# Performance work log

Measured on AMD Instinct MI355X. Metric: run time of the kernel, lower is better.

## Reference

```python
import jax, jax.numpy as jnp
import numpy as np

TAU = 0.07
COS_EPS = 1e-8   # torch F.cosine_similarity eps
L1_EPS = 1e-12   # torch F.normalize eps
MM_EPS = 1e-8    # min-max renorm eps

B, C, H, W = 64, 256, 32, 32
S, D = 512, 256


def setup_inputs() -> dict:
    key = jax.random.key(0)
    k1, k2, k3, k4 = jax.random.split(key, 4)
    scale = 1.0 / np.sqrt(D)
    return {
        "image_patches": jax.random.normal(k1, (B, C, H, W), dtype=jnp.float32),
        "text_tokens": jax.random.normal(k2, (B, S, D), dtype=jnp.float32),
        "Wv": jax.random.normal(k3, (D, D), dtype=jnp.float32) * scale,
        "bv": jnp.zeros((D,), dtype=jnp.float32),
        "Wt": jax.random.normal(k4, (D, D), dtype=jnp.float32) * scale,
        "bt": jnp.zeros((D,), dtype=jnp.float32),
    }


def _linear(x, Wgt, b):
    return x @ Wgt.T + b


def _l2n(x, axis=-1):
    n = jnp.maximum(jnp.linalg.norm(x, axis=axis, keepdims=True), COS_EPS)
    return x / n


def _sym_ce_diag(sim):
    # sim [..., N, N]; mean of -log_softmax diagonals along both class axes
    lsm_r = jax.nn.log_softmax(sim, axis=-1)
    lsm_c = jax.nn.log_softmax(sim, axis=-2)
    d_r = jnp.diagonal(lsm_r, axis1=-2, axis2=-1)
    d_c = jnp.diagonal(lsm_c, axis1=-2, axis2=-1)
    return 0.5 * (-jnp.mean(d_r) - jnp.mean(d_c))


def reference(image_patches, text_tokens, Wv, bv, Wt, bt):
    b, c, h, w = image_patches.shape
    hw = h * w
    # b c h w -> b (h w) c, then adapters
    patches = image_patches.reshape(b, c, hw).transpose(0, 2, 1)  # [b, hw, c]
    patches = _linear(patches, Wv, bv)          # [b, hw, d]
    tokens = _linear(text_tokens, Wt, bt)       # [b, s, d]

    # global embeddings: mean-pool then adapter (adapter applied twice on vision path)
    g_img = _linear(jnp.mean(patches, axis=1), Wv, bv)  # [b, d]
    g_txt = _linear(jnp.mean(tokens, axis=1), Wt, bt)   # [b, d]

    # global contrastive loss (cosine sim / tau, symmetric CE over batch)
    g_sim = (_l2n(g_img) @ _l2n(g_txt).T) / TAU         # [b, b]
    global_loss = _sym_ce_diag(g_sim)

    # fine-grained alignment
    sim = jnp.einsum('bpd,bsd->bps', patches, tokens)   # [b, hw, s]
    mn = jnp.min(sim, axis=1, keepdims=True)
    mx = jnp.max(sim, axis=1, keepdims=True)
    sim = (sim - mn) / (mx - mn + MM_EPS)
    sigma = 1.0 / hw
    sim = jnp.where(sim < sigma, 0.0, sim)
    # L1 normalize over patch dim (torch F.normalize p=1 dim=1)
    weights = sim / jnp.maximum(jnp.sum(jnp.abs(sim), axis=1, keepdims=True), L1_EPS)
    lgve = jnp.einsum('bps,bpd->bsd', weights, patches)  # [b, s, d]

    # fine-grained contrastive loss: cosine sim between grouped-vision and text tokens
    f_sim = jnp.einsum('bid,bjd->bij', _l2n(lgve), _l2n(tokens)) / TAU  # [b, s, s]
    fine_loss = _sym_ce_diag(f_sim)

    return global_loss + fine_loss
```

## Files before the change

kernel.cpp:

```cpp
#include <hip/hip_runtime.h>
#include <math.h>

#define BB   64
#define HWP  1024
#define SS   512
#define DD   256
#define TAU_INV (1.0f/0.07f)
#define SIGMA   (1.0f/1024.0f)

typedef unsigned short us;
typedef __attribute__((ext_vector_type(8))) short short8v;
typedef __attribute__((ext_vector_type(8))) unsigned short ushort8v;
typedef __attribute__((ext_vector_type(4))) float floatx4;

__device__ __forceinline__ float bf2f(us u) {
    return __uint_as_float((unsigned)u << 16);
}
__device__ __forceinline__ us f2bf(float f) {
    unsigned u = __float_as_uint(f);
    u += 0x7FFFu + ((u >> 16) & 1u);
    return (us)(u >> 16);
}
__device__ __forceinline__ void split_bf(float v, us& h, us& l) {
    h = f2bf(v);
    l = f2bf(v - bf2f(h));
}

__device__ __forceinline__ void dma16(const us* g, us* l) {
    __builtin_amdgcn_global_load_lds(
        (const __attribute__((address_space(1))) unsigned int*)g,
        (__attribute__((address_space(3))) unsigned int*)l, 16, 0, 0);
}

__global__ void zero_out_k(float* out) { if (threadIdx.x == 0) out[0] = 0.0f; }

enum { OPM_F32_ROW = 0, OPM_F32_COL = 1, OPM_SPL_ROW = 2, OPM_SPL_COL = 3,
       OPM_B16_COL = 4, OPM_B16_ROW = 5, OPM_WGT_COL = 6, OPM_WGT_ROW = 7 };
enum { OUT_F32 = 0, OUT_B16 = 1 };

#define LDSTRIDE 40

template<int MODE, int ROWS, int NW>
struct SRegs {
    static constexpr int RR = ROWS / 128;
    static constexpr bool ISF32 = (MODE == OPM_F32_ROW) || (MODE == OPM_F32_COL);
    ushort8v h[ISF32 ? 1 : RR][2];
    ushort8v l[(MODE == OPM_SPL_ROW) ? RR : 1][2];
    float4   f[ISF32 ? RR : 1][4];
};

template<int MODE, int ROWS, int NW>
__device__ __forceinline__ void stage_load(
    const char* p0, const char* p1, int ld, int row0, int k0, int tid,
    SRegs<MODE, ROWS, NW>& R)
{
    #pragma unroll
    for (int rr = 0; rr < ROWS / 128; ++rr) {
        if constexpr (MODE == OPM_SPL_ROW) {
            const us* ph = (const us*)p0;
            const us* pl = (const us*)p1;
            if constexpr (NW == 4) {
                const int i = rr * 128 + (tid >> 1), ko = (tid & 1) * 16;
                const long long g = (long long)(row0 + i) * ld + k0 + ko;
                R.h[rr][0] = *(const ushort8v*)&ph[g];
                R.h[rr][1] = *(const ushort8v*)&ph[g + 8];
                R.l[rr][0] = *(const ushort8v*)&pl[g];
                R.l[rr][1] = *(const ushort8v*)&pl[g + 8];
            } else {
                const int i = rr * 128 + (tid >> 2), ko = (tid & 3) * 8;
                const long long g = (long long)(row0 + i) * ld + k0 + ko;
                R.h[rr][0] = *(const ushort8v*)&ph[g];
                R.l[rr][0] = *(const ushort8v*)&pl[g];
            }
        } else if constexpr (MODE == OPM_B16_ROW || MODE == OPM_WGT_ROW) {
            const us* ph = (const us*)p0;
            if constexpr (NW == 4) {
                const int i = rr * 128 + (tid >> 1), ko = (tid & 1) * 16;
                const long long g = (long long)(row0 + i) * ld + k0 + ko;
                R.h[rr][0] = *(const ushort8v*)&ph[g];
                R.h[rr][1] = *(const ushort8v*)&ph[g + 8];
            } else {
                const int i = rr * 128 + (tid >> 2), ko = (tid & 3) * 8;
                const long long g = (long long)(row0 + i) * ld + k0 + ko;
                R.h[rr][0] = *(const ushort8v*)&ph[g];
            }
        } else if constexpr (MODE == OPM_F32_ROW) {
            const float* pf = (const float*)p0;
            if constexpr (NW == 4) {
                const int i = rr * 128 + (tid >> 1), ko = (tid & 1) * 16;
                const long long g = (long long)(row0 + i) * ld + k0 + ko;
                #pragma unroll
                for (int c = 0; c < 4; ++c)
                    R.f[rr][c] = *(const float4*)&pf[g + c * 4];
            } else {
                const int i = rr * 128 + (tid >> 2), ko = (tid & 3) * 8;
                const long long g = (long long)(row0 + i) * ld + k0 + ko;
                R.f[rr][0] = *(const float4*)&pf[g];
                R.f[rr][1] = *(const float4*)&pf[g + 4];
            }
        } else if constexpr (MODE == OPM_F32_COL) {
            const float* pf = (const float*)p0;
            if constexpr (NW == 4) {
                const int m = rr * 128 + (tid & 127), kh = (tid >> 7) * 16;
                const long long base = (long long)(k0 + kh) * ld + row0 + m;
                #pragma unroll
                for (int c = 0; c < 4; ++c) {
                    float4 v;
                    v.x = pf[base + (long long)(c * 4 + 0) * ld];
                    v.y = pf[base + (long long)(c * 4 + 1) * ld];
                    v.z = pf[base + (long long)(c * 4 + 2) * ld];
                    v.w = pf[base + (long long)(c * 4 + 3) * ld];
                    R.f[rr][c] = v;
                }
            } else {
                const int m = rr * 128 + (tid & 127), kh = (tid >> 7) * 8;
                const long long base = (long long)(k0 + kh) * ld + row0 + m;
                #pragma unroll
                for (int c = 0; c < 2; ++c) {
                    float4 v;
                    v.x = pf[base + (long long)(c * 4 + 0) * ld];
                    v.y = pf[base + (long long)(c * 4 + 1) * ld];
                    v.z = pf[base + (long long)(c * 4 + 2) * ld];
                    v.w = pf[base + (long long)(c * 4 + 3) * ld];
                    R.f[rr][c] = v;
                }
            }
        } else if constexpr (MODE == OPM_B16_COL) {
            const us* ph = (const us*)p0;
            if constexpr (NW == 4) {
                const int m = rr * 128 + (tid & 127), kh = (tid >> 7) * 16;
                const long long base = (long long)(k0 + kh) * ld + row0 + m;
                #pragma unroll
                for (int kk = 0; kk < 8; ++kk) {
                    R.h[rr][0][kk] = ph[base + (long long)kk * ld];
                    R.h[rr][1][kk] = ph[base + (long long)(kk + 8) * ld];
                }
            } else {
                const int m = rr * 128 + (tid & 127), kh = (tid >> 7) * 8;
                const long long base = (long long)(k0 + kh) * ld + row0 + m;
                #pragma unroll
                for (int kk = 0; kk < 8; ++kk)
                    R.h[rr][0][kk] = ph[base + (long long)kk * ld];
            }
        }
    }
}

template<int MODE, int ROWS, int NW>
__device__ __forceinline__ void stage_store(
    const SRegs<MODE, ROWS, NW>& R, us* ldsH, us* ldsL, int tid, float nlo, float inv)
{
    #pragma unroll
    for (int rr = 0; rr < ROWS / 128; ++rr) {
        if constexpr (MODE == OPM_SPL_ROW) {
            if constexpr (NW == 4) {
                const int i = rr * 128 + (tid >> 1), ko = (tid & 1) * 16;
                *(ushort8v*)&ldsH[i * LDSTRIDE + ko]     = R.h[rr][0];
                *(ushort8v*)&ldsH[i * LDSTRIDE + ko + 8] = R.h[rr][1];
                *(ushort8v*)&ldsL[i * LDSTRIDE + ko]     = R.l[rr][0];
                *(ushort8v*)&ldsL[i * LDSTRIDE + ko + 8] = R.l[rr][1];
            } else {
                const int i = rr * 128 + (tid >> 2), ko = (tid & 3) * 8;
                *(ushort8v*)&ldsH[i * LDSTRIDE + ko] = R.h[rr][0];
                *(ushort8v*)&ldsL[i * LDSTRIDE + ko] = R.l[rr][0];
            }
        } else if constexpr (MODE == OPM_B16_ROW) {
            if constexpr (NW == 4) {
                const int i = rr * 128 + (tid >> 1), ko = (tid & 1) * 16;
                *(ushort8v*)&ldsH[i * LDSTRIDE + ko]     = R.h[rr][0];
                *(ushort8v*)&ldsH[i * LDSTRIDE + ko + 8] = R.h[rr][1];
            } else {
                const int i = rr * 128 + (tid >> 2), ko = (tid & 3) * 8;
                *(ushort8v*)&ldsH[i * LDSTRIDE + ko] = R.h[rr][0];
            }
        } else if constexpr (MODE == OPM_WGT_ROW) {
            const int i = tid >> 2, ko = (tid & 3) * 8;
            us v[8];
            #pragma unroll
            for (int j = 0; j < 8; ++j) {
                const float w0 = fmaf(bf2f(R.h[0][0][j]), inv, nlo);
                v[j] = (w0 < SIGMA) ? (us)0 : f2bf(w0);
            }
            *(ushort8v*)&ldsH[i * LDSTRIDE + ko] = *(const ushort8v*)&v[0];
        } else if constexpr (MODE == OPM_F32_ROW) {
            if constexpr (NW == 4) {
                const int i = rr * 128 + (tid >> 1), ko = (tid & 1) * 16;
                us h16[16], l16a[16];
                #pragma unroll
                for (int c = 0; c < 4; ++c) {
                    float4 v = R.f[rr][c];
                    split_bf(v.x, h16[c*4+0], l16a[c*4+0]);
                    split_bf(v.y, h16[c*4+1], l16a[c*4+1]);
                    split_bf(v.z, h16[c*4+2], l16a[c*4+2]);
                    split_bf(v.w, h16[c*4+3], l16a[c*4+3]);
                }
                *(ushort8v*)&ldsH[i * LDSTRIDE + ko]     = *(const ushort8v*)&h16[0];
                *(ushort8v*)&ldsH[i * LDSTRIDE + ko + 8] = *(const ushort8v*)&h16[8];
                *(ushort8v*)&ldsL[i * LDSTRIDE + ko]     = *(const ushort8v*)&l16a[0];
                *(ushort8v*)&ldsL[i * LDSTRIDE + ko + 8] = *(const ushort8v*)&l16a[8];
            } else {
                const int i = rr * 128 + (tid >> 2), ko = (tid & 3) * 8;
                us h8[8], l8[8];
                #pragma unroll
                for (int c = 0; c < 2; ++c) {
                    float4 v = R.f[rr][c];
                    split_bf(v.x, h8[c*4+0], l8[c*4+0]);
                    split_bf(v.y, h8[c*4+1], l8[c*4+1]);
                    split_bf(v.z, h8[c*4+2], l8[c*4+2]);
                    split_bf(v.w, h8[c*4+3], l8[c*4+3]);
                }
                *(ushort8v*)&ldsH[i * LDSTRIDE + ko] = *(const ushort8v*)&h8[0];
                *(ushort8v*)&ldsL[i * LDSTRIDE + ko] = *(const ushort8v*)&l8[0];
            }
        } else if constexpr (MODE == OPM_F32_COL) {
            if constexpr (NW == 4) {
                const int m = rr * 128 + (tid & 127), kh = (tid >> 7) * 16;
                us vh[16], vl[16];
                #pragma unroll
                for (int c = 0; c < 4; ++c) {
                    float4 v = R.f[rr][c];
                    split_bf(v.x, vh[c*4+0], vl[c*4+0]);
                    split_bf(v.y, vh[c*4+1], vl[c*4+1]);
                    split_bf(v.z, vh[c*4+2], vl[c*4+2]);
                    split_bf(v.w, vh[c*4+3], vl[c*4+3]);
                }
                *(ushort8v*)&ldsH[m * LDSTRIDE + kh]     = *(const ushort8v*)&vh[0];
                *(ushort8v*)&ldsH[m * LDSTRIDE + kh + 8] = *(const ushort8v*)&vh[8];
                *(ushort8v*)&ldsL[m * LDSTRIDE + kh]     = *(const ushort8v*)&vl[0];
                *(ushort8v*)&ldsL[m * LDSTRIDE + kh + 8] = *(const ushort8v*)&vl[8];
            } else {
                const int m = rr * 128 + (tid & 127), kh = (tid >> 7) * 8;
                us vh[8], vl[8];
                #pragma unroll
                for (int c = 0; c < 2; ++c) {
                    float4 v = R.f[rr][c];
                    split_bf(v.x, vh[c*4+0], vl[c*4+0]);
                    split_bf(v.y, vh[c*4+1], vl[c*4+1]);
                    split_bf(v.z, vh[c*4+2], vl[c*4+2]);
                    split_bf(v.w, vh[c*4+3], vl[c*4+3]);
                }
                *(ushort8v*)&ldsH[m * LDSTRIDE + kh] = *(const ushort8v*)&vh[0];
                *(ushort8v*)&ldsL[m * LDSTRIDE + kh] = *(const ushort8v*)&vl[0];
            }
        } else if constexpr (MODE == OPM_B16_COL) {
            if constexpr (NW == 4) {
                const int m = rr * 128 + (tid & 127), kh = (tid >> 7) * 16;
                us v[16];
                #pragma unroll
                for (int kk = 0; kk < 16; ++kk)
                    v[kk] = (kk < 8) ? R.h[rr][0][kk & 7] : R.h[rr][1][kk & 7];
                *(ushort8v*)&ldsH[m * LDSTRIDE + kh]     = *(const ushort8v*)&v[0];
                *(ushort8v*)&ldsH[m * LDSTRIDE + kh + 8] = *(const ushort8v*)&v[8];
            } else {
                const int m = rr * 128 + (tid & 127), kh = (tid >> 7) * 8;
                *(ushort8v*)&ldsH[m * LDSTRIDE + kh] = R.h[rr][0];
            }
        }
    }
}

template<int AMODE, int BMODE, int OMODE, int EPI, int NT, int PREF, int NW, int DMA>
__global__ __launch_bounds__(NW * 64) void mfma_gemm(
    const void* A0, const void* A1, const void* B0, const void* B1, void* C0,
    int M, int N, int K, int lda, int ldb, int ldc,
    long long sA, long long sB, long long sC,
    const float* __restrict__ bias, const float* __restrict__ invm,
    const float* __restrict__ invn, float scale,
    const float* __restrict__ wlo, const float* __restrict__ whi,
    float* __restrict__ aux0, float* __restrict__ aux1,
    float* __restrict__ aux2, float* __restrict__ aux3, float* __restrict__ aux4)
{
    constexpr bool ASPL = (AMODE <= OPM_SPL_COL);
    constexpr bool BSPL = (BMODE <= OPM_SPL_COL);
    constexpr int NF = NT / 16;
    constexpr int MI = 8 / NW;
    constexpr int RPW = 128 / NW;
    __shared__ __align__(16) us Ah[(DMA == 1) ? 8 : 128 * LDSTRIDE];
    __shared__ __align__(16) us Al[(!DMA && ASPL) ? 128 * LDSTRIDE : 8];
    __shared__ __align__(16) us Bh[DMA ? 8 : NT * LDSTRIDE];
    __shared__ __align__(16) us Bl[(!DMA && BSPL) ? NT * LDSTRIDE : 8];
    __shared__ __align__(16) us AhD[(DMA == 1) ? 2 * 128 * 32 : 8];
    __shared__ __align__(16) us BhD[DMA ? 2 * NT * 32 : 8];
    __shared__ float redm[(EPI == 4) ? NW * NT : 1];
    __shared__ float reds[(EPI == 4) ? NW * NT : 1];

    const int tid = threadIdx.x;
    const int w = tid >> 6, lane = tid & 63;
    const int quad = lane >> 4, l16 = lane & 15;

    int bx = blockIdx.x, by = blockIdx.y, bz = blockIdx.z;
    {
        const int nbx = gridDim.x, nby = gridDim.y, nbz = gridDim.z;
        const int nwg = nbx * nby * nbz;
        if ((nwg & 7) == 0) {
            const int hw = bx + nbx * (by + nby * bz);
            const int cpx = nwg >> 3;
            int wk = (hw & 7) * cpx + (hw >> 3);
            bx = wk % nbx; wk /= nbx;
            by = wk % nby; bz = wk / nby;
        }
    }

    const int m0 = bx * 128, n0 = by * NT;
    const int b = bz;

    const char* Ab0 = (const char*)A0 + (long long)b * sA;
    const char* Ab1 = A1 ? (const char*)A1 + (long long)b * sA : nullptr;
    const char* Bb0 = (const char*)B0 + (long long)b * sB;
    const char* Bb1 = B1 ? (const char*)B1 + (long long)b * sB : nullptr;

    floatx4 acc[MI][NF];
    #pragma unroll
    for (int mi = 0; mi < MI; ++mi)
        #pragma unroll
        for (int ni = 0; ni < NF; ++ni)
            acc[mi][ni] = (floatx4){0.f, 0.f, 0.f, 0.f};

    if constexpr (DMA == 1) {
        const us* Abu = (const us*)Ab0;
        const us* Bbu = (const us*)Bb0;
        const int drow = 16 * w + (lane >> 2);
        const int dcol = (lane & 3) * 8;
        const us* aS = Abu + (long long)(m0 + drow) * lda + dcol;
        const us* bS = Bbu + (long long)(n0 + drow) * ldb + dcol;
        us* aD = &AhD[0] + 512 * w;
        us* bD = &BhD[0] + 512 * w;
        const int NTL = K >> 5;

        dma16(aS,      aD);
        dma16(bS,      bD);
        dma16(aS + 32, aD + 128 * 32);
        dma16(bS + 32, bD + NT * 32);

        int cur = 0;
        for (int t = 0; t < NTL; ++t) {
            if (t + 1 == NTL) asm volatile("s_waitcnt vmcnt(0)" ::: "memory");
            else              asm volatile("s_waitcnt vmcnt(2)" ::: "memory");
            __builtin_amdgcn_s_barrier();
            asm volatile("" ::: "memory");

            {
                const us* Ac = &AhD[cur * 128 * 32];
                const us* Bc = &BhD[cur * NT * 32];
                short8v ah = *(const short8v*)&Ac[(16 * w + l16) * 32 + quad * 8];
                #pragma unroll
                for (int ni = 0; ni < NF; ++ni) {
                    short8v bh = *(const short8v*)&Bc[(16 * ni + l16) * 32 + quad * 8];
                    acc[0][ni] = __builtin_amdgcn_mfma_f32_16x16x32_bf16(ah, bh, acc[0][ni], 0, 0, 0);
                }
            }

            asm volatile("" ::: "memory");
            __builtin_amdgcn_s_barrier();
            if (t + 2 < NTL) {
                const long long off = (long long)(t + 2) * 32;
                dma16(aS + off, aD + cur * 128 * 32);
                dma16(bS + off, bD + cur * NT * 32);
            }
            cur ^= 1;
        }
    } else if constexpr (DMA == 2) {
        const us* Abu = (const us*)Ab0;
        const us* Bbu = (const us*)Bb0;
        const float* wloA = wlo + (long long)b * M;
        const float* whiA = whi + (long long)b * M;
        const int ai = tid >> 2, ako = (tid & 3) * 8;
        const float lo = wloA[m0 + ai];
        const float invA = 1.0f / (whiA[m0 + ai] - lo + 1e-8f);
        const float nloA = -lo * invA;

        const int rB = 16 * w + (lane >> 2);
        const us* bS = Bbu + (long long)(n0 + rB) * ldb + (lane & 3) * 8;
        us* bD = &BhD[0] + 512 * w;
        const long long aRow = (long long)(m0 + ai) * lda + ako;
        const int NTL = K >> 5;

        dma16(bS, bD);
        ushort8v ra = *(const ushort8v*)&Abu[aRow];
        dma16(bS + 32, bD + 4096);

        int cur = 0;
        for (int t = 0; t < NTL; ++t) {
            us v[8];
            #pragma unroll
            for (int j = 0; j < 8; ++j) {
                const float w0 = fmaf(bf2f(ra[j]), invA, nloA);
                v[j] = (w0 < SIGMA) ? (us)0 : f2bf(w0);
            }
            *(ushort8v*)&Ah[ai * LDSTRIDE + ako] = *(const ushort8v*)&v[0];
            asm volatile("s_waitcnt vmcnt(1) lgkmcnt(0)" ::: "memory");
            __builtin_amdgcn_s_barrier();

            if (t + 1 < NTL)
                ra = *(const ushort8v*)&Abu[aRow + (long long)(t + 1) * 32];

            {
                const us* Bc = &BhD[cur * 4096];
                short8v ah = *(const short8v*)&Ah[(16 * w + l16) * LDSTRIDE + quad * 8];
                #pragma unroll
                for (int ni = 0; ni < NF; ++ni) {
                    short8v bh = *(const short8v*)&Bc[(16 * ni + l16) * 32 + quad * 8];
                    acc[0][ni] = __builtin_amdgcn_mfma_f32_16x16x32_bf16(ah, bh, acc[0][ni], 0, 0, 0);
                }
            }
            asm volatile("" ::: "memory");
            __builtin_amdgcn_s_barrier();
            if (t + 2 < NTL)
                dma16(bS + (long long)(t + 2) * 32, bD + cur * 4096);
            cur ^= 1;
        }
    } else {
        float nloA = 0.f, invA = 0.f;
        if constexpr (AMODE == OPM_WGT_ROW) {
            const float* wloA = wlo + (long long)b * M;
            const float* whiA = whi + (long long)b * M;
            const int row = m0 + (tid >> 2);
            const float lo = wloA[row];
            invA = 1.0f / (whiA[row] - lo + 1e-8f);
            nloA = -lo * invA;
        }

        SRegs<AMODE, 128, NW> RA0, RA1;
        SRegs<BMODE, NT, NW>  RB0, RB1;
        if constexpr (PREF) {
            stage_load<AMODE, 128, NW>(Ab0, Ab1, lda, m0, 0, tid, RA0);
            stage_load<BMODE, NT, NW>(Bb0, Bb1, ldb, n0, 0, tid, RB0);
            stage_load<AMODE, 128, NW>(Ab0, Ab1, lda, m0, 32, tid, RA1);
            stage_load<BMODE, NT, NW>(Bb0, Bb1, ldb, n0, 32, tid, RB1);
        }

        auto do_mfma = [&]() {
            short8v ah[MI], al[MI];
            #pragma unroll
            for (int mi = 0; mi < MI; ++mi) {
                const int r = (RPW * w + 16 * mi + l16) * LDSTRIDE + quad * 8;
                ah[mi] = *(const short8v*)&Ah[r];
                if constexpr (ASPL) al[mi] = *(const short8v*)&Al[r];
            }
            #pragma unroll
            for (int ni = 0; ni < NF; ++ni) {
                const int rB = (16 * ni + l16) * LDSTRIDE + quad * 8;
                short8v bh = *(const short8v*)&Bh[rB];
                #pragma unroll
                for (int mi = 0; mi < MI; ++mi)
                    acc[mi][ni] = __builtin_amdgcn_mfma_f32_16x16x32_bf16(ah[mi], bh, acc[mi][ni], 0, 0, 0);
                if constexpr (BSPL) {
                    short8v bl = *(const short8v*)&Bl[rB];
                    #pragma unroll
                    for (int mi = 0; mi < MI; ++mi)
                        acc[mi][ni] = __builtin_amdgcn_mfma_f32_16x16x32_bf16(ah[mi], bl, acc[mi][ni], 0, 0, 0);
                }
                if constexpr (ASPL) {
                    #pragma unroll
                    for (int mi = 0; mi < MI; ++mi)
                        acc[mi][ni] = __builtin_amdgcn_mfma_f32_16x16x32_bf16(al[mi], bh, acc[mi][ni], 0, 0, 0);
                }
            }
        };

#define GEMM_SUBSTEP(RAx, RBx, KCUR, KNEXT)                                    \
    do {                                                                       \
        if constexpr (!PREF) {                                                 \
            stage_load<AMODE, 128, NW>(Ab0, Ab1, lda, m0, (KCUR), tid, RAx);   \
            stage_load<BMODE, NT, NW>(Bb0, Bb1, ldb, n0, (KCUR), tid, RBx);    \
        }                                                                      \
        stage_store<AMODE, 128, NW>(RAx, Ah, Al, tid, nloA, invA);             \
        stage_store<BMODE, NT, NW>(RBx, Bh, Bl, tid, 0.f, 0.f);                \
        if constexpr (PREF) {                                                  \
            asm volatile("s_waitcnt lgkmcnt(0)" ::: "memory");                 \
            __builtin_amdgcn_s_barrier();                                      \
            if ((KNEXT) < K) {                                                 \
                stage_load<AMODE, 128, NW>(Ab0, Ab1, lda, m0, (KNEXT), tid, RAx); \
                stage_load<BMODE, NT, NW>(Bb0, Bb1, ldb, n0, (KNEXT), tid, RBx);  \
            }                                                                  \
        } else {                                                               \
            __syncthreads();                                                   \
        }                                                                      \
        do_mfma();                                                             \
        if constexpr (PREF) {                                                  \
            asm volatile("s_waitcnt lgkmcnt(0)" ::: "memory");                 \
            __builtin_amdgcn_s_barrier();                                      \
        } else {                                                               \
            __syncthreads();                                                   \
        }                                                                      \
    } while (0)

        for (int k0 = 0; k0 < K; k0 += 64) {
            GEMM_SUBSTEP(RA0, RB0, k0, k0 + 64);
            GEMM_SUBSTEP(RA1, RB1, k0 + 32, k0 + 96);
        }
#undef GEMM_SUBSTEP
    }

    if constexpr (EPI != 4) {
        char* Cb0 = (char*)C0 + (long long)b * sC;
        #pragma unroll
        for (int mi = 0; mi < MI; ++mi)
            #pragma unroll
            for (int ni = 0; ni < NF; ++ni)
                #pragma unroll
                for (int r = 0; r < 4; ++r) {
                    const int row = m0 + RPW * w + 16 * mi + quad * 4 + r;
                    const int col = n0 + 16 * ni + l16;
                    float v = acc[mi][ni][r];
                    if constexpr (EPI == 1) v += bias[col];
                    const long long idx = (long long)row * ldc + col;
                    if constexpr (OMODE == OUT_F32) ((float*)Cb0)[idx] = v;
                    else                            ((us*)Cb0)[idx] = f2bf(v);
                }
    }

    if constexpr (EPI == 3) {
        #pragma unroll
        for (int r = 0; r < 4; ++r) {
            const int grow = m0 + RPW * w + quad * 4 + r;
            float lo = 1e30f, hi = -1e30f;
            #pragma unroll
            for (int ni = 0; ni < NF; ++ni) {
                const float vr = bf2f(f2bf(acc[0][ni][r]));
                lo = fminf(lo, vr); hi = fmaxf(hi, vr);
            }
            lo = fminf(lo, __shfl_xor(lo, 1)); hi = fmaxf(hi, __shfl_xor(hi, 1));
            lo = fminf(lo, __shfl_xor(lo, 2)); hi = fmaxf(hi, __shfl_xor(hi, 2));
            lo = fminf(lo, __shfl_xor(lo, 4)); hi = fmaxf(hi, __shfl_xor(hi, 4));
            lo = fminf(lo, __shfl_xor(lo, 8)); hi = fmaxf(hi, __shfl_xor(hi, 8));
            if (l16 == 0) {
                const long long o = ((long long)b * M + grow) * 8 + by;
                aux0[o] = lo; aux1[o] = hi;
            }
        }
    }

    if constexpr (EPI == 4) {
        float bn[NF];
        #pragma unroll
        for (int ni = 0; ni < NF; ++ni)
            bn[ni] = invn[(long long)b * N + n0 + 16 * ni + l16] * scale;
        float amv[MI * 4];
        #pragma unroll
        for (int mi = 0; mi < MI; ++mi)
            #pragma unroll
            for (int r = 0; r < 4; ++r)
                amv[mi * 4 + r] = invm[(long long)b * M + m0 + RPW * w + 16 * mi + quad * 4 + r];

        #pragma unroll
        for (int mi = 0; mi < MI; ++mi)
            #pragma unroll
            for (int r = 0; r < 4; ++r) {
                const int grow = m0 + RPW * w + 16 * mi + quad * 4 + r;
                float vv[NF];
                float rm = -1e30f;
                #pragma unroll
                for (int ni = 0; ni < NF; ++ni) {
                    const float v = acc[mi][ni][r] * amv[mi * 4 + r] * bn[ni];
                    vv[ni] = v;
                    rm = fmaxf(rm, v);
                    if (grow == n0 + 16 * ni + l16)
                        aux4[(long long)b * M + grow] = v;
                }
                #pragma unroll
                for (int o = 8; o > 0; o >>= 1) rm = fmaxf(rm, __shfl_xor(rm, o));
                float rs = 0.f;
                #pragma unroll
                for (int ni = 0; ni < NF; ++ni) rs += expf(vv[ni] - rm);
                #pragma unroll
                for (int o = 8; o > 0; o >>= 1) rs += __shfl_xor(rs, o);
                if (l16 == 0) {
                    const long long o = ((long long)b * M + grow) * 4 + by;
                    aux0[o] = rm; aux1[o] = rs;
                }
            }

        #pragma unroll
        for (int ni = 0; ni < NF; ++ni) {
            float va[MI * 4];
            float cm = -1e30f;
            #pragma unroll
            for (int mi = 0; mi < MI; ++mi)
                #pragma unroll
                for (int r = 0; r < 4; ++r) {
                    const float v = acc[mi][ni][r] * amv[mi * 4 + r] * bn[ni];
                    va[mi * 4 + r] = v;
                    cm = fmaxf(cm, v);
                }
            cm = fmaxf(cm, __shfl_xor(cm, 16));
            cm = fmaxf(cm, __shfl_xor(cm, 32));
            float cs = 0.f;
            #pragma unroll
            for (int j = 0; j < MI * 4; ++j) cs += expf(va[j] - cm);
            cs += __shfl_xor(cs, 16);
            cs += __shfl_xor(cs, 32);
            if (quad == 0) {
                redm[w * NT + 16 * ni + l16] = cm;
                reds[w * NT + 16 * ni + l16] = cs;
            }
        }
        __syncthreads();
        if (tid < NT) {
            float m = -1e30f, s = 0.f;
            #pragma unroll
            for (int w4 = 0; w4 < NW; ++w4) {
                const float cm = redm[w4 * NT + tid], cs = reds[w4 * NT + tid];
                const float nm = fmaxf(m, cm);
                s = s * expf(m - nm) + cs * expf(cm - nm);
                m = nm;
            }
            const long long o = ((long long)b * N + n0 + tid) * 4 + bx;
            aux2[o] = m; aux3[o] = s;
        }
    }
}


__global__ __launch_bounds__(256) void transpose_k(
    const us* __restrict__ src, us* __restrict__ dst)
{
    __shared__ us t[64][66];
    const int b = blockIdx.z;
    const int p0 = blockIdx.x * 64, d0 = blockIdx.y * 64;
    const us* s = src + (long long)b * 262144;
    us* d = dst + (long long)b * 262144;
    const int r = threadIdx.x >> 3, c8 = (threadIdx.x & 7) * 8;
    #pragma unroll
    for (int h = 0; h < 64; h += 32)
        *(ushort8v*)&t[r + h][c8] =
            *(const ushort8v*)&s[(long long)(p0 + r + h) * 256 + d0 + c8];
    __syncthreads();
    #pragma unroll
    for (int h = 0; h < 64; h += 32) {
        us v[8];
        #pragma unroll
        for (int j = 0; j < 8; ++j) v[j] = t[c8 + j][r + h];
        *(ushort8v*)&d[(long long)(d0 + r + h) * 1024 + p0 + c8] =
            *(const ushort8v*)&v[0];
    }
}

__global__ __launch_bounds__(256) void convert_w_k(
    const float* Wv, const float* Wt, us* Wvh, us* Wvl, us* Wth, us* Wtl)
{
    const int i = blockIdx.x * 256 + threadIdx.x;
    split_bf(Wv[i], Wvh[i], Wvl[i]);
    split_bf(Wt[i], Wth[i], Wtl[i]);
}

__global__ __launch_bounds__(256) void mean_img_k(
    const float* __restrict__ img, float* __restrict__ mimg)
{
    const int row = blockIdx.x * 4 + (threadIdx.x >> 6);
    const int lane = threadIdx.x & 63;
    const float* p = img + (long long)row * 1024;
    float s = 0.f;
    #pragma unroll
    for (int c = 0; c < 4; ++c) {
        float4 v = *(const float4*)&p[(c * 64 + lane) * 4];
        s += v.x + v.y + v.z + v.w;
    }
    #pragma unroll
    for (int o = 32; o > 0; o >>= 1) s += __shfl_xor(s, o);
    if (lane == 0) mimg[row] = s * (1.0f / 1024.0f);
}

__global__ __launch_bounds__(256) void mean_text_s1(
    const float* __restrict__ text, float* __restrict__ part)
{
    const int b = blockIdx.x, ch = blockIdx.y, k = threadIdx.x;
    const float* p = text + ((long long)b * 512 + ch * 64) * 256 + k;
    float s = 0.f;
    for (int r = 0; r < 64; ++r) s += p[r * 256];
    part[(b * 8 + ch) * 256 + k] = s;
}
__global__ __launch_bounds__(256) void mean_text_s2(
    const float* __restrict__ part, float* __restrict__ mt)
{
    const int b = blockIdx.x, k = threadIdx.x;
    float s = 0.f;
    for (int c = 0; c < 8; ++c) s += part[(b * 8 + c) * 256 + k];
    mt[b * 256 + k] = s * (1.0f / 512.0f);
}

__global__ __launch_bounds__(256) void small_adapter_k(
    const float* __restrict__ x, const float* __restrict__ W,
    const float* __restrict__ bias, float* __restrict__ y)
{
    const int b = blockIdx.x, d = threadIdx.x;
    __shared__ float xs[256];
    xs[d] = x[b * 256 + d];
    __syncthreads();
    const float4* w = (const float4*)(W + (long long)d * 256);
    const float4* xv = (const float4*)xs;
    float s = bias[d];
    #pragma unroll 8
    for (int k = 0; k < 64; ++k) {
        const float4 a = xv[k], ww = w[k];
        s += a.x * ww.x + a.y * ww.y + a.z * ww.z + a.w * ww.w;
    }
    y[b * 256 + d] = s;
}


__global__ __launch_bounds__(256) void inv_norm_f32_k(
    const float* __restrict__ x, float* __restrict__ inv)
{
    const int row = blockIdx.x * 4 + (threadIdx.x >> 6);
    const int lane = threadIdx.x & 63;
    float4 v = *(const float4*)&x[(long long)row * 256 + lane * 4];
    float s = v.x * v.x + v.y * v.y + v.z * v.z + v.w * v.w;
    #pragma unroll
    for (int o = 32; o > 0; o >>= 1) s += __shfl_xor(s, o);
    if (lane == 0) inv[row] = 1.0f / fmaxf(sqrtf(s), 1e-8f);
}

__global__ __launch_bounds__(256) void g_sim_k(
    const float* __restrict__ gi, const float* __restrict__ gt,
    const float* __restrict__ invI, const float* __restrict__ invT,
    float* __restrict__ gs)
{
    const int i = blockIdx.x, t = threadIdx.x;
    const int j = t >> 2, part = t & 3;
    __shared__ float a[256];
    a[t] = gi[i * 256 + t];
    __syncthreads();
    const float* bp = gt + (long long)j * 256 + part * 64;
    const float* ap = a + part * 64;
    float s = 0.f;
    #pragma unroll 16
    for (int k = 0; k < 64; ++k) s += ap[k] * bp[k];
    s += __shfl_xor(s, 1);
    s += __shfl_xor(s, 2);
    if (part == 0) gs[i * 64 + j] = s * invI[i] * invT[j] * TAU_INV;
}

__global__ __launch_bounds__(64) void g_lse_k(
    const float* __restrict__ gs, float* __restrict__ out)
{
    const int b = blockIdx.x, lane = threadIdx.x;
    const bool is_col = b >= 64;
    const int r = is_col ? b - 64 : b;
    const float v = is_col ? gs[lane * 64 + r] : gs[r * 64 + lane];
    float m = v;
    #pragma unroll
    for (int o = 32; o > 0; o >>= 1) m = fmaxf(m, __shfl_xor(m, o));
    float s = expf(v - m);
    #pragma unroll
    for (int o = 32; o > 0; o >>= 1) s += __shfl_xor(s, o);
    if (lane == 0)
        atomicAdd(out, ((m + logf(s)) - gs[r * 64 + r]) * (0.5f / 64.0f));
}

__global__ __launch_bounds__(256) void inv_norm_b16_k(
    const us* __restrict__ x, float* __restrict__ inv)
{
    const int row = blockIdx.x * 4 + (threadIdx.x >> 6);
    const int lane = threadIdx.x & 63;
    ushort4 h = *(const ushort4*)&x[(long long)row * 256 + lane * 4];
    const float x0 = bf2f(h.x), x1 = bf2f(h.y), x2 = bf2f(h.z), x3 = bf2f(h.w);
    float s = x0 * x0 + x1 * x1 + x2 * x2 + x3 * x3;
    #pragma unroll
    for (int o = 32; o > 0; o >>= 1) s += __shfl_xor(s, o);
    if (lane == 0) inv[row] = 1.0f / fmaxf(sqrtf(s), 1e-8f);
}


__global__ __launch_bounds__(256) void minmax_merge_k(
    const float* __restrict__ mnp, const float* __restrict__ mxp,
    float* __restrict__ mn, float* __restrict__ mx)
{
    const int idx = blockIdx.x * 256 + threadIdx.x;
    float lo = 1e30f, hi = -1e30f;
    #pragma unroll
    for (int c = 0; c < 8; ++c) {
        lo = fminf(lo, mnp[(long long)idx * 8 + c]);
        hi = fmaxf(hi, mxp[(long long)idx * 8 + c]);
    }
    mn[idx] = lo; mx[idx] = hi;
}

__global__ __launch_bounds__(256) void fine_merge4_k(
    const float* __restrict__ pm, const float* __restrict__ ps,
    const float* __restrict__ diag, float* __restrict__ out)
{
    const int idx = blockIdx.x * 256 + threadIdx.x;
    float m = -1e30f, s = 0.f;
    #pragma unroll
    for (int c = 0; c < 4; ++c) {
        const float cm = pm[(long long)idx * 4 + c], cs = ps[(long long)idx * 4 + c];
        const float nm = fmaxf(m, cm);
        s = s * expf(m - nm) + cs * expf(cm - nm);
        m = nm;
    }
    const float contrib = (m + logf(s)) - diag[idx];
    __shared__ float red[256];
    red[threadIdx.x] = contrib;
    __syncthreads();
    for (int w = 128; w > 0; w >>= 1) {
        if (threadIdx.x < w) red[threadIdx.x] += red[threadIdx.x + w];
        __syncthreads();
    }
    if (threadIdx.x == 0) atomicAdd(out, red[0] * (0.5f / (64.0f * 512.0f)));
}

extern "C" void kernel_launch(void* const* d_in, const int* in_sizes, int n_in,
                              void* d_out, int out_size, void* d_ws, size_t ws_size,
                              hipStream_t stream)
{
    const float* img  = (const float*)d_in[0];
    const float* text = (const float*)d_in[1];
    const float* Wv   = (const float*)d_in[2];
    const float* bv   = (const float*)d_in[3];
    const float* Wt   = (const float*)d_in[4];
    const float* bt   = (const float*)d_in[5];
    float* out = (float*)d_out;
    char* ws = (char*)d_ws;

    us* patches = (us*)(ws + 0);
    us* tokens  = (us*)(ws + 33554432);
    us* simT    = (us*)(ws + 50331648);
    us* lgve    = (us*)(ws + 117440512);
    char* st = ws + 134217728;
    float* mean_img  = (float*)(st + 0);
    float* mean_text = (float*)(st + 65536);
    float* mean_pat  = (float*)(st + 131072);
    float* mean_tok  = (float*)(st + 196608);
    float* g_img     = (float*)(st + 262144);
    float* g_txt     = (float*)(st + 327680);
    float* textpart  = (float*)(st + 393216);
    float* mnp       = (float*)(st + 917504);
    float* mxp       = (float*)(st + 1966080);
    float* mnv       = (float*)(st + 3014656);
    float* mxv       = (float*)(st + 3145728);
    float* inv_l     = (float*)(st + 3276800);
    float* inv_t     = (float*)(st + 3407872);
    us* Wvh = (us*)(st + 3538944);
    us* Wvl = (us*)(st + 3670016);
    us* Wth = (us*)(st + 3801088);
    us* Wtl = (us*)(st + 3932160);
    float* inv_gi  = (float*)(st + 4063232);
    float* inv_gt  = (float*)(st + 4063744);
    float* g_simbf = (float*)(st + 4064256);
    float* pm_row  = (float*)(st + 4194304);
    float* ps_row  = (float*)(st + 4718592);
    float* pm_col  = (float*)(st + 5242880);
    float* ps_col  = (float*)(st + 5767168);
    float* diag    = (float*)(st + 6291456);
    us* patchesT   = (us*)(ws + 140640256);

    zero_out_k<<<1, 64, 0, stream>>>(out);
    convert_w_k<<<256, 256, 0, stream>>>(Wv, Wt, Wvh, Wvl, Wth, Wtl);

    mean_img_k<<<4096, 256, 0, stream>>>(img, mean_img);
    mean_text_s1<<<dim3(64, 8), 256, 0, stream>>>(text, textpart);
    mean_text_s2<<<64, 256, 0, stream>>>(textpart, mean_text);
    small_adapter_k<<<BB, 256, 0, stream>>>(mean_img, Wv, bv, mean_pat);
    small_adapter_k<<<BB, 256, 0, stream>>>(mean_pat, Wv, bv, g_img);
    small_adapter_k<<<BB, 256, 0, stream>>>(mean_text, Wt, bt, mean_tok);
    small_adapter_k<<<BB, 256, 0, stream>>>(mean_tok, Wt, bt, g_txt);
    inv_norm_f32_k<<<16, 256, 0, stream>>>(g_img, inv_gi);
    inv_norm_f32_k<<<16, 256, 0, stream>>>(g_txt, inv_gt);
    g_sim_k<<<64, 256, 0, stream>>>(g_img, g_txt, inv_gi, inv_gt, g_simbf);
    g_lse_k<<<128, 64, 0, stream>>>(g_simbf, out);

    mfma_gemm<OPM_F32_COL, OPM_SPL_ROW, OUT_B16, 1, 256, 0, 8, 0><<<dim3(8, 1, BB), 512, 0, stream>>>(
        img, nullptr, Wvh, Wvl, patches,
        1024, 256, 256, 1024, 256, 256,
        1048576LL, 0LL, 524288LL, bv, nullptr, nullptr, 0.f, nullptr, nullptr,
        nullptr, nullptr, nullptr, nullptr, nullptr);

    mfma_gemm<OPM_F32_ROW, OPM_SPL_ROW, OUT_B16, 1, 256, 0, 8, 0><<<dim3(4, 1, BB), 512, 0, stream>>>(
        text, nullptr, Wth, Wtl, tokens,
        512, 256, 256, 256, 256, 256,
        524288LL, 0LL, 262144LL, bt, nullptr, nullptr, 0.f, nullptr, nullptr,
        nullptr, nullptr, nullptr, nullptr, nullptr);

    transpose_k<<<dim3(16, 4, BB), 256, 0, stream>>>(patches, patchesT);

    mfma_gemm<OPM_B16_ROW, OPM_B16_ROW, OUT_B16, 3, 128, 0, 8, 1><<<dim3(4, 8, BB), 512, 0, stream>>>(
        tokens, nullptr, patches, nullptr, simT,
        512, 1024, 256, 256, 256, 1024,
        262144LL, 524288LL, 1048576LL, nullptr, nullptr, nullptr, 0.f, nullptr, nullptr,
        mnp, mxp, nullptr, nullptr, nullptr);

    minmax_merge_k<<<128, 256, 0, stream>>>(mnp, mxp, mnv, mxv);

    mfma_gemm<OPM_WGT_ROW, OPM_B16_COL, OUT_B16, 0, 128, 0, 8, 2><<<dim3(4, 2, BB), 512, 0, stream>>>(
        simT, nullptr, patchesT, nullptr, lgve,
        512, 256, 1024, 1024, 1024, 256,
        1048576LL, 524288LL, 262144LL, nullptr, nullptr, nullptr, 0.f, mnv, mxv,
        nullptr, nullptr, nullptr, nullptr, nullptr);

    inv_norm_b16_k<<<8192, 256, 0, stream>>>(lgve, inv_l);
    inv_norm_b16_k<<<8192, 256, 0, stream>>>(tokens, inv_t);

    mfma_gemm<OPM_B16_ROW, OPM_B16_ROW, OUT_B16, 4, 128, 0, 8, 1><<<dim3(4, 4, BB), 512, 0, stream>>>(
        lgve, nullptr, tokens, nullptr, nullptr,
        512, 512, 256, 256, 256, 512,
        262144LL, 262144LL, 0LL, nullptr, inv_l, inv_t, TAU_INV, nullptr, nullptr,
        pm_row, ps_row, pm_col, ps_col, diag);

    fine_merge4_k<<<128, 256, 0, stream>>>(pm_row, ps_row, diag, out);
    fine_merge4_k<<<128, 256, 0, stream>>>(pm_col, ps_col, diag, out);
}
```

Baseline: 378.3 us.

## Pre-split adapter inputs to bf16 hi/lo and stream via async DMA GEMM

```diff
diff --git a/kernel.cpp b/kernel.cpp
--- a/kernel.cpp
+++ b/kernel.cpp
@@ -275,12 +275,14 @@
     constexpr int NF = NT / 16;
     constexpr int MI = 8 / NW;
     constexpr int RPW = 128 / NW;
-    __shared__ __align__(16) us Ah[(DMA == 1) ? 8 : 128 * LDSTRIDE];
+    __shared__ __align__(16) us Ah[(DMA == 1 || DMA == 3) ? 8 : 128 * LDSTRIDE];
     __shared__ __align__(16) us Al[(!DMA && ASPL) ? 128 * LDSTRIDE : 8];
     __shared__ __align__(16) us Bh[DMA ? 8 : NT * LDSTRIDE];
     __shared__ __align__(16) us Bl[(!DMA && BSPL) ? NT * LDSTRIDE : 8];
-    __shared__ __align__(16) us AhD[(DMA == 1) ? 2 * 128 * 32 : 8];
+    __shared__ __align__(16) us AhD[(DMA == 1 || DMA == 3) ? 2 * 128 * 32 : 8];
     __shared__ __align__(16) us BhD[DMA ? 2 * NT * 32 : 8];
+    __shared__ __align__(16) us AlD[(DMA == 3) ? 2 * 128 * 32 : 8];
+    __shared__ __align__(16) us BlD[(DMA == 3) ? 2 * NT * 32 : 8];
     __shared__ float redm[(EPI == 4) ? NW * NT : 1];
     __shared__ float reds[(EPI == 4) ? NW * NT : 1];
 
@@ -407,6 +409,64 @@
             __builtin_amdgcn_s_barrier();
             if (t + 2 < NTL)
                 dma16(bS + (long long)(t + 2) * 32, bD + cur * 4096);
+            cur ^= 1;
+        }
+    } else if constexpr (DMA == 3) {
+        const us* AhU = (const us*)Ab0;
+        const us* AlU = (const us*)Ab1;
+        const us* BhU = (const us*)Bb0;
+        const us* BlU = (const us*)Bb1;
+        const int drow = 16 * w + (lane >> 2);
+        const int dcol = (lane & 3) * 8;
+        const us* aHS = AhU + (long long)(m0 + drow) * lda + dcol;
+        const us* aLS = AlU + (long long)(m0 + drow) * lda + dcol;
+        const us* bHS = BhU + (long long)(n0 + drow) * ldb + dcol;
+        const us* bLS = BlU + (long long)(n0 + drow) * ldb + dcol;
+        us* aHDp = &AhD[0] + 512 * w;
+        us* aLDp = &AlD[0] + 512 * w;
+        us* bHDp = &BhD[0] + 512 * w;
+        us* bLDp = &BlD[0] + 512 * w;
+        const int NTL = K >> 5;
+
+        dma16(aHS, aHDp); dma16(aLS, aLDp); dma16(bHS, bHDp); dma16(bLS, bLDp);
+        dma16(aHS + 32, aHDp + 4096); dma16(aLS + 32, aLDp + 4096);
+        dma16(bHS + 32, bHDp + 4096); dma16(bLS + 32, bLDp + 4096);
+
+        int cur = 0;
+        for (int t = 0; t < NTL; ++t) {
+            if (t + 1 == NTL) asm volatile("s_waitcnt vmcnt(0)" ::: "memory");
+            else              asm volatile("s_waitcnt vmcnt(4)" ::: "memory");
+            __builtin_amdgcn_s_barrier();
+            asm volatile("" ::: "memory");
+
+            {
+                const us* Ach = &AhD[cur * 4096];
+                const us* Acl = &AlD[cur * 4096];
+                const us* Bch = &BhD[cur * 4096];
+                const us* Bcl = &BlD[cur * 4096];
+                const int ra = (16 * w + l16) * 32 + quad * 8;
+                short8v ah = *(const short8v*)&Ach[ra];
+                short8v al = *(const short8v*)&Acl[ra];
+                #pragma unroll
+                for (int ni = 0; ni < NF; ++ni) {
+                    const int rb = (16 * ni + l16) * 32 + quad * 8;
+                    short8v bh = *(const short8v*)&Bch[rb];
+                    short8v bl = *(const short8v*)&Bcl[rb];
+                    acc[0][ni] = __builtin_amdgcn_mfma_f32_16x16x32_bf16(ah, bh, acc[0][ni], 0, 0, 0);
+                    acc[0][ni] = __builtin_amdgcn_mfma_f32_16x16x32_bf16(ah, bl, acc[0][ni], 0, 0, 0);
+                    acc[0][ni] = __builtin_amdgcn_mfma_f32_16x16x32_bf16(al, bh, acc[0][ni], 0, 0, 0);
+                }
+            }
+
+            asm volatile("" ::: "memory");
+            __builtin_amdgcn_s_barrier();
+            if (t + 2 < NTL) {
+                const long long off = (long long)(t + 2) * 32;
+                dma16(aHS + off, aHDp + cur * 4096);
+                dma16(aLS + off, aLDp + cur * 4096);
+                dma16(bHS + off, bHDp + cur * 4096);
+                dma16(bLS + off, bLDp + cur * 4096);
+            }
             cur ^= 1;
         }
     } else {
@@ -634,6 +694,46 @@
         *(ushort8v*)&d[(long long)(d0 + r + h) * 1024 + p0 + c8] =
             *(const ushort8v*)&v[0];
     }
+}
+
+__global__ __launch_bounds__(256) void convsplit_img_k(
+    const float* __restrict__ img, us* __restrict__ th, us* __restrict__ tl)
+{
+    __shared__ float t[64][65];
+    const int b = blockIdx.z;
+    const int p0 = blockIdx.x * 64, c0 = blockIdx.y * 64;
+    const float* s = img + (long long)b * 262144;
+    const int r = threadIdx.x >> 4, c4 = (threadIdx.x & 15) * 4;
+    #pragma unroll
+    for (int h = 0; h < 64; h += 16) {
+        float4 v = *(const float4*)&s[(long long)(c0 + r + h) * 1024 + p0 + c4];
+        t[r + h][c4 + 0] = v.x; t[r + h][c4 + 1] = v.y;
+        t[r + h][c4 + 2] = v.z; t[r + h][c4 + 3] = v.w;
+    }
+    __syncthreads();
+    #pragma unroll
+    for (int h = 0; h < 64; h += 16) {
+        const int p = h + r;
+        us vh[4], vl[4];
+        #pragma unroll
+        for (int j = 0; j < 4; ++j)
+            split_bf(t[c4 + j][p], vh[j], vl[j]);
+        const long long o = (long long)b * 262144 + (long long)(p0 + p) * 256 + c0 + c4;
+        *(ushort4*)&th[o] = *(const ushort4*)&vh[0];
+        *(ushort4*)&tl[o] = *(const ushort4*)&vl[0];
+    }
+}
+
+__global__ __launch_bounds__(256) void convsplit_row_k(
+    const float* __restrict__ x, us* __restrict__ th, us* __restrict__ tl)
+{
+    const long long i = ((long long)blockIdx.x * 256 + threadIdx.x) * 4;
+    float4 v = *(const float4*)&x[i];
+    us vh[4], vl[4];
+    split_bf(v.x, vh[0], vl[0]); split_bf(v.y, vh[1], vl[1]);
+    split_bf(v.z, vh[2], vl[2]); split_bf(v.w, vh[3], vl[3]);
+    *(ushort4*)&th[i] = *(const ushort4*)&vh[0];
+    *(ushort4*)&tl[i] = *(const ushort4*)&vl[0];
 }
 
 __global__ __launch_bounds__(256) void convert_w_k(
@@ -844,6 +944,10 @@
     float* ps_col  = (float*)(st + 5767168);
     float* diag    = (float*)(st + 6291456);
     us* patchesT   = (us*)(ws + 140640256);
+    us* imgTH = (us*)(ws + 50331648);
+    us* imgTL = (us*)(ws + 83886080);
+    us* textH = (us*)(ws + 140640256);
+    us* textL = (us*)(ws + 157417472);
 
     zero_out_k<<<1, 64, 0, stream>>>(out);
     convert_w_k<<<256, 256, 0, stream>>>(Wv, Wt, Wvh, Wvl, Wth, Wtl);
@@ -860,16 +964,19 @@
     g_sim_k<<<64, 256, 0, stream>>>(g_img, g_txt, inv_gi, inv_gt, g_simbf);
     g_lse_k<<<128, 64, 0, stream>>>(g_simbf, out);
 
-    mfma_gemm<OPM_F32_COL, OPM_SPL_ROW, OUT_B16, 1, 256, 0, 8, 0><<<dim3(8, 1, BB), 512, 0, stream>>>(
-        img, nullptr, Wvh, Wvl, patches,
-        1024, 256, 256, 1024, 256, 256,
-        1048576LL, 0LL, 524288LL, bv, nullptr, nullptr, 0.f, nullptr, nullptr,
+    convsplit_img_k<<<dim3(16, 4, BB), 256, 0, stream>>>(img, imgTH, imgTL);
+    convsplit_row_k<<<8192, 256, 0, stream>>>(text, textH, textL);
+
+    mfma_gemm<OPM_B16_ROW, OPM_B16_ROW, OUT_B16, 1, 128, 0, 8, 3><<<dim3(8, 2, BB), 512, 0, stream>>>(
+        imgTH, imgTL, Wvh, Wvl, patches,
+        1024, 256, 256, 256, 256, 256,
+        524288LL, 0LL, 524288LL, bv, nullptr, nullptr, 0.f, nullptr, nullptr,
         nullptr, nullptr, nullptr, nullptr, nullptr);
 
-    mfma_gemm<OPM_F32_ROW, OPM_SPL_ROW, OUT_B16, 1, 256, 0, 8, 0><<<dim3(4, 1, BB), 512, 0, stream>>>(
-        text, nullptr, Wth, Wtl, tokens,
+    mfma_gemm<OPM_B16_ROW, OPM_B16_ROW, OUT_B16, 1, 128, 0, 8, 3><<<dim3(4, 2, BB), 512, 0, stream>>>(
+        textH, textL, Wth, Wtl, tokens,
         512, 256, 256, 256, 256, 256,
-        524288LL, 0LL, 262144LL, bt, nullptr, nullptr, 0.f, nullptr, nullptr,
+        262144LL, 0LL, 262144LL, bt, nullptr, nullptr, 0.f, nullptr, nullptr,
         nullptr, nullptr, nullptr, nullptr, nullptr);
 
     transpose_k<<<dim3(16, 4, BB), 256, 0, stream>>>(patches, patchesT);
```

Result: slower. 403.1 us (+6.6%).
